# Kernel optimization log

Hardware: AMD Instinct MI355X
Metric: run time of the kernel (lower is better)

Reference implementation:

```python
import jax, jax.numpy as jnp
from jax import lax
import numpy as np

WAY = 100
SHOT = 5
QUERY = 15
D = 4096
LAM = 10.0
ALPHA = 0.2
N_EPOCHS = 20
EPS = 1e-6
MAXITERS = 1000
N_L = WAY * SHOT          # 500 labeled
N_U = WAY * QUERY         # 1500 unlabeled
N_TOT = N_L + N_U         # 2000


def setup_inputs() -> dict:
    key = jax.random.key(0)
    kx, = jax.random.split(key, 1)
    X = jax.random.uniform(kx, (N_TOT, D), dtype=jnp.float32)  # features must be >= 0
    # data is ordered as (shot+query) blocks of `way` samples, one per class
    labels = jnp.tile(jnp.arange(WAY, dtype=jnp.int32), SHOT + QUERY)
    return {"X": X, "labels": labels}


def _normalize(X):
    # F.normalize(p=2, dim=-1) with eps=1e-12
    return X / jnp.maximum(jnp.linalg.norm(X, axis=-1, keepdims=True), 1e-12)


def _cdist(X, Y):
    # Euclidean distances [n, m] via gram trick (avoids [n, m, d] intermediate)
    d2 = (X * X).sum(-1)[:, None] + (Y * Y).sum(-1)[None, :] - 2.0 * (X @ Y.T)
    return jnp.sqrt(jnp.maximum(d2, 1e-12))


def _sinkhorn(M, r, c):
    # Row/col scaling loop of compute_optimal_transport, tracked via scaling
    # vectors (a, b) so P_k = a * K * b exactly matches the in-place updates.
    K = jnp.exp(-LAM * M)
    K = K / K.sum()
    n, m = M.shape

    def step(carry, _):
        a, b, prev, done = carry
        rowsum = a * (K @ b)                       # P.sum(-1)
        err = jnp.max(jnp.abs(prev - rowsum))      # convergence check vs old u
        done = done | (err <= EPS)
        a_new = jnp.where(done, a, a * r / rowsum)
        colsum = b * (K.T @ a_new)                 # P.sum(1) after row scaling
        b_new = jnp.where(done, b, b * c / colsum)
        prev_new = jnp.where(done, prev, rowsum)
        return (a_new, b_new, prev_new, done), None

    init = (jnp.ones(n, M.dtype), jnp.ones(m, M.dtype),
            jnp.zeros(n, M.dtype), jnp.array(False))
    (a, b, _, _), _ = lax.scan(step, init, None, length=MAXITERS)
    return a[:, None] * K * b[None, :]


def _forward(X, labels):
    # power transform
    X = jnp.sqrt(X + 1e-6)
    # scale (mode='val'): normalize -> center labeled/unlabeled separately -> normalize
    X = _normalize(X)
    Xl = X[:N_L] - X[:N_L].mean(0, keepdims=True)
    Xu = X[N_L:] - X[N_L:].mean(0, keepdims=True)
    Z = _normalize(jnp.concatenate([Xl, Xu], axis=0))

    # init class means from labeled shots
    mus0 = Z.reshape(SHOT + QUERY, WAY, -1)[:SHOT].mean(0)  # [way, d]

    r = jnp.ones(N_U, Z.dtype)
    c = jnp.full((WAY,), float(QUERY), Z.dtype)
    onehot = jax.nn.one_hot(labels[:N_L], WAY, dtype=Z.dtype)

    def get_probas(mus):
        dist = _cdist(Z, mus)                      # [n_tot, way]
        Pu = _sinkhorn(dist[N_L:], r, c)           # [n_u, way]
        return jnp.concatenate([onehot, Pu], axis=0)

    def epoch(mus, _):
        p = get_probas(mus)
        emus = (p.T @ Z) / p.sum(0)[:, None]       # estimate_from_mask
        return mus + ALPHA * (emus - mus), None    # update_from_estimate

    mus, _ = lax.scan(epoch, mus0, None, length=N_EPOCHS)

    P = get_probas(mus)
    logP = jnp.log(P[N_L:] + 1e-5)
    acc = (jnp.argmax(P[N_L:], axis=-1) == labels[N_L:]).astype(jnp.float32).mean()
    return logP, acc


def reference(X, labels):
    return _forward(X, labels)
```

## Files before the change

### kernel.cpp

```cpp
#include <hip/hip_runtime.h>

#define WAY   100
#define SHOT  5
#define NQ    15
#define DD    4096
#define N_L   500
#define N_U   1500
#define N_TOT 2000
#define LAMF  10.0f
#define EPSF  1e-6f
#define MAXIT 1000

#define OFF_Z      0u
#define OFF_CPP    3145728u
#define OFF_MEANL  8192000u
#define OFF_MEANU  8196096u
#define OFF_SL     8200192u
#define OFF_MUSA   8609792u
#define OFF_MUSB   9068544u
#define OFF_MUSQP  9527296u
#define OFF_MUSB16 9552896u
#define OFF_PTH    9782272u
#define OFF_PTL    9868288u
#define OFF_KMAT   9954304u
#define OFF_COLS   10104320u
#define OFF_MISC   10113920u
#define OFF_ZUT    10114688u
#define OFF_ZUTL   13260416u
#define OFF_AG     16406144u
#define OFF_PREVG  16407680u
#define OFF_BINIT  16409216u

#define SINK_BLOCKS 8
#define SINK_T 512
#define RPB 188
#define KLS 101
#define PTS 1536
#define CPS 409600u

typedef __attribute__((ext_vector_type(8))) short short8_t;
typedef __attribute__((ext_vector_type(4))) float f32x4;

__device__ __forceinline__ short f2bs(float f) {
  unsigned u = __float_as_uint(f);
  unsigned r = (u + 0x7FFFu + ((u >> 16) & 1u)) >> 16;
  return (short)r;
}
__device__ __forceinline__ float bs2f(short s) {
  return __uint_as_float(((unsigned)(unsigned short)s) << 16);
}

__device__ __forceinline__ float ld_agent(const float* p) {
  return __hip_atomic_load(p, __ATOMIC_RELAXED, __HIP_MEMORY_SCOPE_AGENT);
}
__device__ __forceinline__ void st_agent(float* p, float v) {
  __hip_atomic_store(p, v, __ATOMIC_RELAXED, __HIP_MEMORY_SCOPE_AGENT);
}

__global__ __launch_bounds__(256) void k_pow_norm(const float* __restrict__ X, float* __restrict__ Z,
                                                  float* __restrict__ msums, unsigned* __restrict__ misc_u,
                                                  float* __restrict__ aG) {
  int i = blockIdx.x, tid = threadIdx.x;
  __shared__ float red[256];
  if (i < 32) msums[i * 256 + tid] = 0.f;
  if (i == 32) { misc_u[tid] = 0u; misc_u[tid + 256] = 0u; misc_u[tid + 512] = 0u; }
  if (i == 33) { for (int z = tid; z < 1504; z += 256) aG[z] = -1.f; }
  const float* x = X + (size_t)i * DD;
  float s = 0.f;
  for (int k = tid; k < DD; k += 256) s += x[k] + 1e-6f;
  red[tid] = s; __syncthreads();
  for (int o = 128; o > 0; o >>= 1) { if (tid < o) red[tid] += red[tid + o]; __syncthreads(); }
  float inv = 1.0f / fmaxf(sqrtf(red[0]), 1e-12f);
  float* z = Z + (size_t)i * DD;
  for (int k = tid; k < DD; k += 256) z[k] = sqrtf(x[k] + 1e-6f) * inv;
}

__global__ __launch_bounds__(256) void k_colmeans(const float* __restrict__ Z, float* __restrict__ mLs,
                                                  float* __restrict__ mUs) {
  int k = blockIdx.x * 256 + threadIdx.x;
  int r0 = blockIdx.y * 80;
  float sL = 0.f, sU = 0.f;
  for (int r = r0; r < r0 + 80; ++r) {
    float v = Z[(size_t)r * DD + k];
    if (r < N_L) sL += v; else sU += v;
  }
  if (r0 < N_L) atomicAdd(&mLs[k], sL);
  if (r0 + 80 > N_L) atomicAdd(&mUs[k], sU);
}

__global__ __launch_bounds__(256) void k_center(float* __restrict__ Z, const float* __restrict__ mLs,
                                                const float* __restrict__ mUs) {
  int i = blockIdx.x, tid = threadIdx.x;
  __shared__ float red[256];
  const float* m = (i < N_L) ? mLs : mUs;
  const float scale = (i < N_L) ? (1.0f / 500.0f) : (1.0f / 1500.0f);
  float* z = Z + (size_t)i * DD;
  float s = 0.f;
  for (int k = tid; k < DD; k += 256) { float v = z[k] - m[k] * scale; s += v * v; }
  red[tid] = s; __syncthreads();
  for (int o = 128; o > 0; o >>= 1) { if (tid < o) red[tid] += red[tid + o]; __syncthreads(); }
  float inv = 1.0f / fmaxf(sqrtf(red[0]), 1e-12f);
  for (int k = tid; k < DD; k += 256) z[k] = (z[k] - m[k] * scale) * inv;
}

__global__ __launch_bounds__(256) void k_musinit(const float* __restrict__ Z, float* __restrict__ SL,
                                                 float* __restrict__ mus, short* __restrict__ musb,
                                                 float* __restrict__ musqP, float* __restrict__ binit) {
  int w = blockIdx.x, tid = threadIdx.x;
  __shared__ float red[256];
  if (tid == 0) binit[w] = 1.0f;
  float q = 0.f;
  for (int k = tid; k < DD; k += 256) {
    float s = 0.f;
    for (int sh = 0; sh < SHOT; ++sh) s += Z[(size_t)(sh * WAY + w) * DD + k];
    SL[(size_t)w * DD + k] = s;
    float m = s / 5.0f;
    mus[(size_t)w * DD + k] = m;
    musb[(size_t)w * DD + k] = f2bs(m);
    q += m * m;
  }
  red[tid] = q; __syncthreads();
  for (int o = 128; o > 0; o >>= 1) { if (tid < o) red[tid] += red[tid + o]; __syncthreads(); }
  if (tid == 0) musqP[(size_t)w * 256] = red[0];
  else musqP[(size_t)w * 256 + tid] = 0.f;
}

__global__ __launch_bounds__(256) void k_zb(const float* __restrict__ Z, short* __restrict__ Zb, int ubase) {
  size_t i0 = (size_t)ubase * DD + ((size_t)blockIdx.x * 256 + threadIdx.x) * 8;
  short8_t v;
  if (i0 < (size_t)N_U * DD) {
    const float* src = Z + (size_t)N_L * DD + i0;
    float4 a = *(const float4*)src;
    float4 b = *(const float4*)(src + 4);
    v[0] = f2bs(a.x); v[1] = f2bs(a.y); v[2] = f2bs(a.z); v[3] = f2bs(a.w);
    v[4] = f2bs(b.x); v[5] = f2bs(b.y); v[6] = f2bs(b.z); v[7] = f2bs(b.w);
  } else {
    v = (short8_t){0, 0, 0, 0, 0, 0, 0, 0};
  }
  *(short8_t*)(Zb + i0) = v;
}

__global__ __launch_bounds__(256) void k_zt(const float* __restrict__ Z, short* __restrict__ ZTH,
                                            short* __restrict__ ZTL) {
  __shared__ float tile[32][33];
  int k0 = blockIdx.x * 32, u0 = blockIdx.y * 32;
  int c = threadIdx.x & 31, r0 = threadIdx.x >> 5;
#pragma unroll
  for (int rr = 0; rr < 4; ++rr) {
    int r = r0 + rr * 8;
    int u = u0 + r;
    tile[r][c] = (u < N_U) ? Z[(size_t)(N_L + u) * DD + k0 + c] : 0.f;
  }
  __syncthreads();
#pragma unroll
  for (int rr = 0; rr < 4; ++rr) {
    int r = r0 + rr * 8;
    float v = tile[c][r];
    short hi = f2bs(v);
    ZTH[(size_t)(k0 + r) * PTS + u0 + c] = hi;
    ZTL[(size_t)(k0 + r) * PTS + u0 + c] = f2bs(v - bs2f(hi));
  }
}

__global__ __launch_bounds__(256) void k_gemm1K(const short* __restrict__ Zb, const short* __restrict__ musb,
                                                const float* __restrict__ musqP, float* __restrict__ Kmat,
                                                unsigned* __restrict__ misc_u) {
  int tid = threadIdx.x;
  __shared__ float redA[4 * 7 * 4 * 64];
  __shared__ float musq2[2][128];
  if (blockIdx.x == 0) {
    for (int z = tid; z < 768; z += 256) misc_u[z] = 0u;
  }
  {
    int w = tid >> 1, half = tid & 1;
    if (w < WAY) {
      const float* mp = musqP + (size_t)w * 256 + half * 128;
      float q = 0.f;
#pragma unroll 4
      for (int bb = 0; bb < 128; bb += 4) {
        float4 v4 = *(const float4*)(mp + bb);
        q += (v4.x + v4.y) + (v4.z + v4.w);
      }
      musq2[half][w] = q;
    }
  }
  int wv = tid >> 6, l = tid & 63;
  int l15 = l & 15, quad = (l >> 4) & 3;
  int u0 = blockIdx.x * 16;
  f32x4 acc[7];
#pragma unroll
  for (int c = 0; c < 7; ++c) acc[c] = (f32x4){0.f, 0.f, 0.f, 0.f};

  const short* bp = Zb + (size_t)(u0 + l15) * DD + wv * 1024 + quad * 8;
  const short* ap = musb + (size_t)l15 * DD + wv * 1024 + quad * 8;
#pragma unroll 2
  for (int kc = 0; kc < 1024; kc += 32) {
    short8_t bf = *(const short8_t*)(bp + kc);
#pragma unroll
    for (int c = 0; c < 7; ++c) {
      short8_t af = *(const short8_t*)(ap + (size_t)c * 16 * DD + kc);
      acc[c] = __builtin_amdgcn_mfma_f32_16x16x32_bf16(af, bf, acc[c], 0, 0, 0);
    }
  }
#pragma unroll
  for (int c = 0; c < 7; ++c)
#pragma unroll
    for (int r = 0; r < 4; ++r)
      redA[((wv * 7 + c) * 4 + r) * 64 + l] = acc[c][r];
  __syncthreads();
  if (wv == 0) {
    int u = u0 + l15;
#pragma unroll
    for (int c = 0; c < 7; ++c)
#pragma unroll
      for (int r = 0; r < 4; ++r) {
        int base = (c * 4 + r) * 64 + l;
        float s = redA[base] + redA[base + 1792] + redA[base + 3584] + redA[base + 5376];
        int w = 16 * c + quad * 4 + r;
        if (w < WAY && u < N_U) {
          float d2 = 1.0f + (musq2[0][w] + musq2[1][w]) - 2.0f * s;
          Kmat[(size_t)u * WAY + w] = expf(-LAMF * sqrtf(fmaxf(d2, 1e-12f)));
        }
      }
  }
}

__device__ __forceinline__ void gbar(unsigned* slots, unsigned t) {
  __syncthreads();
  if (threadIdx.x == 0) {
    asm volatile("s_waitcnt vmcnt(0) lgkmcnt(0)" ::: "memory");
    __hip_atomic_store(slots + (unsigned)blockIdx.x * 16, t, __ATOMIC_RELAXED, __HIP_MEMORY_SCOPE_AGENT);
  }
  if (threadIdx.x < SINK_BLOCKS) {
    while (__hip_atomic_load(slots + threadIdx.x * 16, __ATOMIC_RELAXED, __HIP_MEMORY_SCOPE_AGENT) < t)
      __builtin_amdgcn_s_sleep(1);
  }
  __syncthreads();
}

__global__ __launch_bounds__(SINK_T) void k_sink(const float* __restrict__ Kg,
                                                 short* __restrict__ PTH, short* __restrict__ PTL,
                                                 float* __restrict__ colsP, float* __restrict__ aG,
                                                 float* __restrict__ prevG, float* __restrict__ binit,
                                                 unsigned* __restrict__ misc_u, float* __restrict__ misc_f) {
  __shared__ float Kl[RPB * KLS];
  __shared__ float a[RPB], aold[RPB], prevs[RPB], b[WAY];
  __shared__ float rerr[SINK_T];
  __shared__ float c2[5 * WAY];
  __shared__ float red[SINK_T];
  __shared__ float eSh;
  unsigned* slots = misc_u + 8;
  float* KsumG = misc_f + 3;
  int tid = threadIdx.x;
  int row0 = blockIdx.x * RPB;
  int nrows = (row0 + RPB <= N_U) ? RPB : (N_U - row0);

  float ks = 0.f;
  for (int idx = tid; idx < nrows * WAY; idx += SINK_T) {
    float v = Kg[row0 * WAY + idx];
    int r = idx / WAY, j = idx - r * WAY;
    Kl[r * KLS + j] = v;
    ks += v;
  }
  red[tid] = ks; __syncthreads();
  for (int o = SINK_T / 2; o > 0; o >>= 1) { if (tid < o) red[tid] += red[tid + o]; __syncthreads(); }
  if (tid == 0) atomicAdd(KsumG, red[0]);
  if (tid < WAY) b[tid] = binit[tid];

  bool warm = (aG[row0] >= 0.f);
  unsigned bt = 0;
  if (!warm) { ++bt; gbar(slots, bt); }
  float S = warm ? 1.f : ld_agent(KsumG);
  if (tid < RPB) {
    a[tid] = warm ? aG[row0 + tid] : (1.0f / S);
    prevs[tid] = warm ? prevG[row0 + tid] : 0.f;
  }

  bool conv = false;
  for (int t = 0; t < MAXIT; ++t) {
    float* cp = colsP + (t & 1) * 4096;
    __syncthreads();
    if (tid < nrows) {
      const float* kr = &Kl[tid * KLS];
      float r0 = 0.f, r1 = 0.f, r2 = 0.f, r3 = 0.f;
#pragma unroll 4
      for (int j = 0; j < WAY; j += 4) {
        r0 = fmaf(kr[j], b[j], r0);
        r1 = fmaf(kr[j + 1], b[j + 1], r1);
        r2 = fmaf(kr[j + 2], b[j + 2], r2);
        r3 = fmaf(kr[j + 3], b[j + 3], r3);
      }
      float rs = ((r0 + r1) + (r2 + r3)) * a[tid];
      rerr[tid] = fabsf(prevs[tid] - rs);
      aold[tid] = a[tid];
      a[tid] = a[tid] / rs;
      prevs[tid] = rs;
    } else {
      rerr[tid] = 0.f;
    }
    __syncthreads();
    if (tid < 500) {
      int slot = tid / 100;
      int j = tid - slot * 100;
      int rlo = slot * 38;
      int rhi = rlo + 38; if (rhi > nrows) rhi = nrows;
      float pc = 0.f;
      for (int r = rlo; r < rhi; ++r) pc = fmaf(Kl[r * KLS + j], a[r], pc);
      c2[slot * WAY + j] = pc;
    }
    __syncthreads();
    if (tid < WAY) {
      float s0 = c2[tid] + c2[WAY + tid] + c2[2 * WAY + tid] + c2[3 * WAY + tid] + c2[4 * WAY + tid];
      st_agent(cp + (unsigned)blockIdx.x * 128 + tid, s0);
    }
    if (tid < 64) {
      float m = rerr[tid];
#pragma unroll
      for (int k = 1; k < 8; ++k) m = fmaxf(m, rerr[tid + 64 * k]);
#pragma unroll
      for (int o = 32; o > 0; o >>= 1) m = fmaxf(m, __shfl_down(m, o));
      if (tid == 0) st_agent(cp + (unsigned)blockIdx.x * 128 + 100, m);
    }
    ++bt;
    gbar(slots, bt);
    float bnew = 0.f;
    if (tid >= 256 && tid < 256 + WAY) {
      int j = tid - 256;
      float s = 0.f;
#pragma unroll
      for (int sb = 0; sb < SINK_BLOCKS; ++sb) s += ld_agent(cp + sb * 128 + j);
      bnew = (float)NQ / s;
    }
    if (tid < 64) {
      float e = (tid < SINK_BLOCKS) ? ld_agent(cp + tid * 128 + 100) : 0.f;
#pragma unroll
      for (int o = 4; o > 0; o >>= 1) e = fmaxf(e, __shfl_down(e, o));
      if (tid == 0) eSh = e;
    }
    __syncthreads();
    if (eSh <= EPSF) { conv = true; break; }
    if (tid >= 256 && tid < 256 + WAY) b[tid - 256] = bnew;
  }
  __syncthreads();
  if (tid < nrows) {
    float af = conv ? aold[tid] : a[tid];
    aG[row0 + tid] = af;
    prevG[row0 + tid] = prevs[tid];
  }
  if (blockIdx.x == 0 && tid < WAY) binit[tid] = b[tid];
  for (int idx = tid; idx < WAY * nrows; idx += SINK_T) {
    int j = idx / nrows; int r = idx - j * nrows;
    float av = conv ? aold[r] : a[r];
    float p = av * Kl[r * KLS + j] * b[j];
    short hi = f2bs(p);
    PTH[(size_t)j * PTS + row0 + r] = hi;
    PTL[(size_t)j * PTS + row0 + r] = f2bs(p - bs2f(hi));
  }
  if (blockIdx.x == SINK_BLOCKS - 1) {
    for (int idx = tid; idx < WAY * 4; idx += SINK_T) {
      int j = idx >> 2;
      PTH[(size_t)j * PTS + 1500 + (idx & 3)] = 0;
      PTL[(size_t)j * PTS + 1500 + (idx & 3)] = 0;
    }
  }
}

__global__ __launch_bounds__(64) void k_gemm2(const short* __restrict__ PTH, const short* __restrict__ PTL,
                                              const short* __restrict__ ZTH, const short* __restrict__ ZTL,
                                              float* __restrict__ CPp) {
  int l = threadIdx.x, l15 = l & 15, quad = l >> 4;
  int k0 = blockIdx.x * 16;
  int us = blockIdx.y;
  int kcb = us * 192;
  int kce = (us == 7) ? 1504 : kcb + 192;
  f32x4 acc[7];
#pragma unroll
  for (int c = 0; c < 7; ++c) acc[c] = (f32x4){0.f, 0.f, 0.f, 0.f};
  size_t aoff = (size_t)l15 * PTS + quad * 8;
  const short* bph = ZTH + (size_t)(k0 + l15) * PTS + quad * 8;
  const short* bpl = ZTL + (size_t)(k0 + l15) * PTS + quad * 8;
  for (int kc = kcb; kc < kce; kc += 32) {
    short8_t bh = *(const short8_t*)(bph + kc);
    short8_t bl = *(const short8_t*)(bpl + kc);
#pragma unroll
    for (int c = 0; c < 7; ++c) {
      short8_t ah = *(const short8_t*)(PTH + aoff + (size_t)c * 16 * PTS + kc);
      short8_t al = *(const short8_t*)(PTL + aoff + (size_t)c * 16 * PTS + kc);
      acc[c] = __builtin_amdgcn_mfma_f32_16x16x32_bf16(ah, bh, acc[c], 0, 0, 0);
      acc[c] = __builtin_amdgcn_mfma_f32_16x16x32_bf16(al, bh, acc[c], 0, 0, 0);
      acc[c] = __builtin_amdgcn_mfma_f32_16x16x32_bf16(ah, bl, acc[c], 0, 0, 0);
    }
  }
  float* dst = CPp + (size_t)us * CPS;
#pragma unroll
  for (int c = 0; c < 7; ++c)
#pragma unroll
    for (int r = 0; r < 4; ++r) {
      int w = 16 * c + quad * 4 + r;
      if (w < WAY) dst[(size_t)w * DD + k0 + l15] = acc[c][r];
    }
}

__global__ __launch_bounds__(256) void k_musup(const float* __restrict__ musR, const float* __restrict__ SL,
                                               const float* __restrict__ CPp, float* __restrict__ musW,
                                               short* __restrict__ musb, float* __restrict__ musqP) {
  int w = blockIdx.x, tid = threadIdx.x;
  int kb = blockIdx.y * 1024;
  __shared__ float red[256];
  float q = 0.f;
  for (int k = kb + tid; k < kb + 1024; k += 256) {
    size_t o = (size_t)w * DD + k;
    float c = 0.f;
#pragma unroll
    for (int s = 0; s < 8; ++s) c += CPp[(size_t)s * CPS + o];
    float emus = (SL[o] + c) / 20.0f;
    float m = musR[o];
    float v = m + 0.2f * (emus - m);
    musW[o] = v;
    musb[o] = f2bs(v);
    q += v * v;
  }
  red[tid] = q; __syncthreads();
  for (int o = 128; o > 0; o >>= 1) { if (tid < o) red[tid] += red[tid + o]; __syncthreads(); }
  if (tid == 0) musqP[(size_t)w * 256 + blockIdx.y] = red[0];
}

__global__ __launch_bounds__(128) void k_final(const short* __restrict__ PTH, const short* __restrict__ PTL,
                                               const int* __restrict__ labels, float* __restrict__ out,
                                               unsigned* __restrict__ ctr) {
  int u = blockIdx.x, tid = threadIdx.x;
  __shared__ float vals[WAY];
  if (tid < WAY) {
    float v = bs2f(PTH[(size_t)tid * PTS + u]) + bs2f(PTL[(size_t)tid * PTS + u]);
    vals[tid] = v;
    out[(size_t)u * WAY + tid] = logf(v + 1e-5f);
  }
  __syncthreads();
  if (tid == 0) {
    int am = 0; float bv = vals[0];
    for (int j = 1; j < WAY; ++j) { if (vals[j] > bv) { bv = vals[j]; am = j; } }
    if (am == labels[N_L + u]) atomicAdd(ctr, 1u);
  }
}

__global__ void k_acc(const unsigned* __restrict__ ctr, float* __restrict__ out) {
  if (threadIdx.x == 0) out[N_U * WAY] = (float)(*ctr) / 1500.0f;
}

extern "C" void kernel_launch(void* const* d_in, const int* in_sizes, int n_in,
                              void* d_out, int out_size, void* d_ws, size_t ws_size,
                              hipStream_t stream) {
  const float* X = (const float*)d_in[0];
  const int* labels = (const int*)d_in[1];
  float* out = (float*)d_out;
  float* ws = (float*)d_ws;

  float* Z     = ws + OFF_Z;
  short* Zb    = (short*)(ws + OFF_Z);
  float* CPp   = ws + OFF_CPP;
  float* meanL = ws + OFF_MEANL;
  float* meanU = ws + OFF_MEANU;
  float* SL    = ws + OFF_SL;
  float* musA  = ws + OFF_MUSA;
  float* musB  = ws + OFF_MUSB;
  float* musqP = ws + OFF_MUSQP;
  short* musb16 = (short*)(ws + OFF_MUSB16);
  short* PTH   = (short*)(ws + OFF_PTH);
  short* PTL   = (short*)(ws + OFF_PTL);
  float* Kmat  = ws + OFF_KMAT;
  float* colsP = ws + OFF_COLS;
  float* misc_f = ws + OFF_MISC;
  unsigned* misc_u = (unsigned*)(ws + OFF_MISC);
  short* ZTH   = (short*)(ws + OFF_ZUT);
  short* ZTL   = (short*)(ws + OFF_ZUTL);
  float* aG    = ws + OFF_AG;
  float* prevG = ws + OFF_PREVG;
  float* binit = ws + OFF_BINIT;

  k_pow_norm<<<N_TOT, 256, 0, stream>>>(X, Z, meanL, misc_u, aG);
  k_colmeans<<<dim3(16, 25), 256, 0, stream>>>(Z, meanL, meanU);
  k_center<<<N_TOT, 256, 0, stream>>>(Z, meanL, meanU);
  k_musinit<<<WAY, 256, 0, stream>>>(Z, SL, musA, musb16, musqP, binit);
  k_zt<<<dim3(128, 48), 256, 0, stream>>>(Z, ZTH, ZTL);
  k_zb<<<1536, 256, 0, stream>>>(Z, Zb, 0);
  k_zb<<<1536, 256, 0, stream>>>(Z, Zb, 768);

  float* musR = musA;
  float* musW = musB;
  for (int e = 0; e < 20; ++e) {
    k_gemm1K<<<96, 256, 0, stream>>>(Zb, musb16, musqP, Kmat, misc_u);
    k_sink<<<SINK_BLOCKS, SINK_T, 0, stream>>>(Kmat, PTH, PTL, colsP, aG, prevG, binit, misc_u, misc_f);
    k_gemm2<<<dim3(256, 8), 64, 0, stream>>>(PTH, PTL, ZTH, ZTL, CPp);
    k_musup<<<dim3(WAY, 4), 256, 0, stream>>>(musR, SL, CPp, musW, musb16, musqP);
    float* tmp = musR; musR = musW; musW = tmp;
  }
  k_gemm1K<<<96, 256, 0, stream>>>(Zb, musb16, musqP, Kmat, misc_u);
  k_sink<<<SINK_BLOCKS, SINK_T, 0, stream>>>(Kmat, PTH, PTL, colsP, aG, prevG, binit, misc_u, misc_f);
  k_final<<<N_U, 128, 0, stream>>>(PTH, PTL, labels, out, misc_u + 5);
  k_acc<<<1, 64, 0, stream>>>(misc_u + 5, out);
}
```

Before: 2.313 ms.

## Split Sinkhorn over 16 blocks, fuse gemm2 with mus update and final output

The Sinkhorn solver now runs on 16 cooperating blocks of 94 rows instead of 8 blocks of 188, and its inner loops use float4 shared-memory accesses. The split-K GEMM plus separate mus-update kernel is replaced by one full-K MFMA kernel that applies the update and norm partials directly, which removes the CPp partial buffer round trip. The final log/argmax kernel is folded into the last Sinkhorn launch. Using more blocks shortens the per-iteration row work but adds participants to the spin barrier, and the full-K GEMM runs only 256 blocks.

```diff
diff --git a/kernel.cpp b/kernel.cpp
--- a/kernel.cpp
+++ b/kernel.cpp
@@ -12,7 +12,6 @@
 #define MAXIT 1000
 
 #define OFF_Z      0u
-#define OFF_CPP    3145728u
 #define OFF_MEANL  8192000u
 #define OFF_MEANU  8196096u
 #define OFF_SL     8200192u
@@ -31,12 +30,11 @@
 #define OFF_PREVG  16407680u
 #define OFF_BINIT  16409216u
 
-#define SINK_BLOCKS 8
+#define SINK_BLOCKS 16
 #define SINK_T 512
-#define RPB 188
-#define KLS 101
+#define RPB 94
+#define CPR 12
 #define PTS 1536
-#define CPS 409600u
 
 typedef __attribute__((ext_vector_type(8))) short short8_t;
 typedef __attribute__((ext_vector_type(4))) float f32x4;
@@ -232,7 +230,7 @@
     __hip_atomic_store(slots + (unsigned)blockIdx.x * 16, t, __ATOMIC_RELAXED, __HIP_MEMORY_SCOPE_AGENT);
   }
   if (threadIdx.x < SINK_BLOCKS) {
-    while (__hip_atomic_load(slots + threadIdx.x * 16, __ATOMIC_RELAXED, __HIP_MEMORY_SCOPE_AGENT) < t)
+    while (__hip_atomic_load(slots + threadIdx.x * 16, __ATOMIC_ACQUIRE, __HIP_MEMORY_SCOPE_AGENT) < t)
       __builtin_amdgcn_s_sleep(1);
   }
   __syncthreads();
@@ -242,55 +240,60 @@
                                                  short* __restrict__ PTH, short* __restrict__ PTL,
                                                  float* __restrict__ colsP, float* __restrict__ aG,
                                                  float* __restrict__ prevG, float* __restrict__ binit,
-                                                 unsigned* __restrict__ misc_u, float* __restrict__ misc_f) {
-  __shared__ float Kl[RPB * KLS];
-  __shared__ float a[RPB], aold[RPB], prevs[RPB], b[WAY];
+                                                 unsigned* __restrict__ misc_u, float* __restrict__ misc_f,
+                                                 const int* __restrict__ labels, float* __restrict__ out,
+                                                 int finalmode) {
+  __shared__ float Kl[RPB * 100];
+  __shared__ float4 bS4[25];
+  __shared__ float a[RPB], aold[RPB], prevs[RPB];
   __shared__ float rerr[SINK_T];
-  __shared__ float c2[5 * WAY];
+  __shared__ float c2[800];
   __shared__ float red[SINK_T];
   __shared__ float eSh;
+  float* bS = (float*)bS4;
   unsigned* slots = misc_u + 8;
   float* KsumG = misc_f + 3;
   int tid = threadIdx.x;
-  int row0 = blockIdx.x * RPB;
-  int nrows = (row0 + RPB <= N_U) ? RPB : (N_U - row0);
+  int row0 = (int)blockIdx.x * RPB;
+  int nrows = (blockIdx.x == SINK_BLOCKS - 1) ? (N_U - row0) : RPB;
 
   float ks = 0.f;
-  for (int idx = tid; idx < nrows * WAY; idx += SINK_T) {
-    float v = Kg[row0 * WAY + idx];
-    int r = idx / WAY, j = idx - r * WAY;
-    Kl[r * KLS + j] = v;
-    ks += v;
+  int n4 = nrows * 25;
+  const float4* Ksrc = (const float4*)(Kg + (size_t)row0 * 100);
+  for (int i = tid; i < n4; i += SINK_T) {
+    float4 v = Ksrc[i];
+    *(float4*)(&Kl[i * 4]) = v;
+    ks += (v.x + v.y) + (v.z + v.w);
   }
   red[tid] = ks; __syncthreads();
   for (int o = SINK_T / 2; o > 0; o >>= 1) { if (tid < o) red[tid] += red[tid + o]; __syncthreads(); }
   if (tid == 0) atomicAdd(KsumG, red[0]);
-  if (tid < WAY) b[tid] = binit[tid];
+  if (tid < WAY) bS[tid] = binit[tid];
 
   bool warm = (aG[row0] >= 0.f);
   unsigned bt = 0;
   if (!warm) { ++bt; gbar(slots, bt); }
   float S = warm ? 1.f : ld_agent(KsumG);
-  if (tid < RPB) {
+  if (tid < nrows) {
     a[tid] = warm ? aG[row0 + tid] : (1.0f / S);
     prevs[tid] = warm ? prevG[row0 + tid] : 0.f;
   }
 
   bool conv = false;
   for (int t = 0; t < MAXIT; ++t) {
-    float* cp = colsP + (t & 1) * 4096;
+    float* cp = colsP + (t & 1) * 2048;
     __syncthreads();
     if (tid < nrows) {
-      const float* kr = &Kl[tid * KLS];
-      float r0 = 0.f, r1 = 0.f, r2 = 0.f, r3 = 0.f;
-#pragma unroll 4
-      for (int j = 0; j < WAY; j += 4) {
-        r0 = fmaf(kr[j], b[j], r0);
-        r1 = fmaf(kr[j + 1], b[j + 1], r1);
-        r2 = fmaf(kr[j + 2], b[j + 2], r2);
-        r3 = fmaf(kr[j + 3], b[j + 3], r3);
+      const float* kr = &Kl[tid * 100];
+      float4 ac = {0.f, 0.f, 0.f, 0.f};
+#pragma unroll
+      for (int j4 = 0; j4 < 25; ++j4) {
+        float4 bv = bS4[j4];
+        float4 kv = *(const float4*)(kr + j4 * 4);
+        ac.x = fmaf(kv.x, bv.x, ac.x); ac.y = fmaf(kv.y, bv.y, ac.y);
+        ac.z = fmaf(kv.z, bv.z, ac.z); ac.w = fmaf(kv.w, bv.w, ac.w);
       }
-      float rs = ((r0 + r1) + (r2 + r3)) * a[tid];
+      float rs = ((ac.x + ac.y) + (ac.z + ac.w)) * a[tid];
       rerr[tid] = fabsf(prevs[tid] - rs);
       aold[tid] = a[tid];
       a[tid] = a[tid] / rs;
@@ -299,27 +302,32 @@
       rerr[tid] = 0.f;
     }
     __syncthreads();
-    if (tid < 500) {
-      int slot = tid / 100;
-      int j = tid - slot * 100;
-      int rlo = slot * 38;
-      int rhi = rlo + 38; if (rhi > nrows) rhi = nrows;
-      float pc = 0.f;
-      for (int r = rlo; r < rhi; ++r) pc = fmaf(Kl[r * KLS + j], a[r], pc);
-      c2[slot * WAY + j] = pc;
+    if (tid < 200) {
+      int j4 = tid % 25, ch = tid / 25;
+      int rlo = ch * CPR, rhi = rlo + CPR; if (rhi > nrows) rhi = nrows;
+      float4 pa = {0.f, 0.f, 0.f, 0.f};
+      for (int r = rlo; r < rhi; ++r) {
+        float4 kv = *(const float4*)(&Kl[r * 100 + j4 * 4]);
+        float av = a[r];
+        pa.x = fmaf(kv.x, av, pa.x); pa.y = fmaf(kv.y, av, pa.y);
+        pa.z = fmaf(kv.z, av, pa.z); pa.w = fmaf(kv.w, av, pa.w);
+      }
+      *(float4*)(&c2[ch * 100 + j4 * 4]) = pa;
+    }
+    if (tid >= 448) {
+      int t6 = tid & 63;
+      float m = rerr[t6];
+#pragma unroll
+      for (int k = 1; k < 8; ++k) m = fmaxf(m, rerr[t6 + 64 * k]);
+#pragma unroll
+      for (int o = 32; o > 0; o >>= 1) m = fmaxf(m, __shfl_down(m, o));
+      if (t6 == 0) st_agent(cp + (unsigned)blockIdx.x * 128 + 100, m);
     }
     __syncthreads();
     if (tid < WAY) {
-      float s0 = c2[tid] + c2[WAY + tid] + c2[2 * WAY + tid] + c2[3 * WAY + tid] + c2[4 * WAY + tid];
-      st_agent(cp + (unsigned)blockIdx.x * 128 + tid, s0);
-    }
-    if (tid < 64) {
-      float m = rerr[tid];
-#pragma unroll
-      for (int k = 1; k < 8; ++k) m = fmaxf(m, rerr[tid + 64 * k]);
-#pragma unroll
-      for (int o = 32; o > 0; o >>= 1) m = fmaxf(m, __shfl_down(m, o));
-      if (tid == 0) st_agent(cp + (unsigned)blockIdx.x * 128 + 100, m);
+      float s = ((c2[tid] + c2[100 + tid]) + (c2[200 + tid] + c2[300 + tid])) +
+                ((c2[400 + tid] + c2[500 + tid]) + (c2[600 + tid] + c2[700 + tid]));
+      st_agent(cp + (unsigned)blockIdx.x * 128 + tid, s);
     }
     ++bt;
     gbar(slots, bt);
@@ -334,24 +342,41 @@
     if (tid < 64) {
       float e = (tid < SINK_BLOCKS) ? ld_agent(cp + tid * 128 + 100) : 0.f;
 #pragma unroll
-      for (int o = 4; o > 0; o >>= 1) e = fmaxf(e, __shfl_down(e, o));
+      for (int o = 8; o > 0; o >>= 1) e = fmaxf(e, __shfl_down(e, o));
       if (tid == 0) eSh = e;
     }
     __syncthreads();
     if (eSh <= EPSF) { conv = true; break; }
-    if (tid >= 256 && tid < 256 + WAY) b[tid - 256] = bnew;
+    if (tid >= 256 && tid < 256 + WAY) bS[tid - 256] = bnew;
   }
   __syncthreads();
+
+  if (finalmode) {
+    for (int idx = tid; idx < nrows * WAY; idx += SINK_T) {
+      int r = idx / WAY, j = idx - r * WAY;
+      float av = conv ? aold[r] : a[r];
+      float p = av * Kl[r * 100 + j] * bS[j];
+      out[(size_t)(row0 + r) * WAY + j] = logf(p + 1e-5f);
+    }
+    if (tid < nrows) {
+      const float* kr = &Kl[tid * 100];
+      int am = 0; float bv = kr[0] * bS[0];
+      for (int j = 1; j < WAY; ++j) { float p = kr[j] * bS[j]; if (p > bv) { bv = p; am = j; } }
+      if (am == labels[N_L + row0 + tid]) atomicAdd(misc_u + 5, 1u);
+    }
+    return;
+  }
+
   if (tid < nrows) {
     float af = conv ? aold[tid] : a[tid];
     aG[row0 + tid] = af;
     prevG[row0 + tid] = prevs[tid];
   }
-  if (blockIdx.x == 0 && tid < WAY) binit[tid] = b[tid];
+  if (blockIdx.x == 0 && tid < WAY) binit[tid] = bS[tid];
   for (int idx = tid; idx < WAY * nrows; idx += SINK_T) {
     int j = idx / nrows; int r = idx - j * nrows;
     float av = conv ? aold[r] : a[r];
-    float p = av * Kl[r * KLS + j] * b[j];
+    float p = av * Kl[r * 100 + j] * bS[j];
     short hi = f2bs(p);
     PTH[(size_t)j * PTS + row0 + r] = hi;
     PTL[(size_t)j * PTS + row0 + r] = f2bs(p - bs2f(hi));
@@ -365,81 +390,63 @@
   }
 }
 
-__global__ __launch_bounds__(64) void k_gemm2(const short* __restrict__ PTH, const short* __restrict__ PTL,
-                                              const short* __restrict__ ZTH, const short* __restrict__ ZTL,
-                                              float* __restrict__ CPp) {
-  int l = threadIdx.x, l15 = l & 15, quad = l >> 4;
-  int k0 = blockIdx.x * 16;
-  int us = blockIdx.y;
-  int kcb = us * 192;
-  int kce = (us == 7) ? 1504 : kcb + 192;
-  f32x4 acc[7];
-#pragma unroll
-  for (int c = 0; c < 7; ++c) acc[c] = (f32x4){0.f, 0.f, 0.f, 0.f};
-  size_t aoff = (size_t)l15 * PTS + quad * 8;
-  const short* bph = ZTH + (size_t)(k0 + l15) * PTS + quad * 8;
-  const short* bpl = ZTL + (size_t)(k0 + l15) * PTS + quad * 8;
-  for (int kc = kcb; kc < kce; kc += 32) {
+__global__ __launch_bounds__(128) void k_gemm2m(const short* __restrict__ PTH, const short* __restrict__ PTL,
+                                                const short* __restrict__ ZTH, const short* __restrict__ ZTL,
+                                                const float* __restrict__ musR, const float* __restrict__ SL,
+                                                float* __restrict__ musW, short* __restrict__ musb,
+                                                float* __restrict__ musqP) {
+  int tid = threadIdx.x, wv = tid >> 6, l = tid & 63;
+  int l15 = l & 15, quad = (l >> 4) & 3;
+  int k0 = blockIdx.x;
+  int c0 = wv ? 4 : 0, nc = wv ? 3 : 4;
+  __shared__ float sq2[7][16][16];
+  f32x4 acc[4];
+#pragma unroll
+  for (int c = 0; c < 4; ++c) acc[c] = (f32x4){0.f, 0.f, 0.f, 0.f};
+  size_t aoff = (size_t)(c0 * 16 + l15) * PTS + quad * 8;
+  const short* bph = ZTH + (size_t)(k0 * 16 + l15) * PTS + quad * 8;
+  const short* bpl = ZTL + (size_t)(k0 * 16 + l15) * PTS + quad * 8;
+  for (int kc = 0; kc < 1504; kc += 32) {
     short8_t bh = *(const short8_t*)(bph + kc);
     short8_t bl = *(const short8_t*)(bpl + kc);
 #pragma unroll
-    for (int c = 0; c < 7; ++c) {
-      short8_t ah = *(const short8_t*)(PTH + aoff + (size_t)c * 16 * PTS + kc);
-      short8_t al = *(const short8_t*)(PTL + aoff + (size_t)c * 16 * PTS + kc);
-      acc[c] = __builtin_amdgcn_mfma_f32_16x16x32_bf16(ah, bh, acc[c], 0, 0, 0);
-      acc[c] = __builtin_amdgcn_mfma_f32_16x16x32_bf16(al, bh, acc[c], 0, 0, 0);
-      acc[c] = __builtin_amdgcn_mfma_f32_16x16x32_bf16(ah, bl, acc[c], 0, 0, 0);
-    }
-  }
-  float* dst = CPp + (size_t)us * CPS;
-#pragma unroll
-  for (int c = 0; c < 7; ++c)
-#pragma unroll
-    for (int r = 0; r < 4; ++r) {
-      int w = 16 * c + quad * 4 + r;
-      if (w < WAY) dst[(size_t)w * DD + k0 + l15] = acc[c][r];
-    }
-}
-
-__global__ __launch_bounds__(256) void k_musup(const float* __restrict__ musR, const float* __restrict__ SL,
-                                               const float* __restrict__ CPp, float* __restrict__ musW,
-                                               short* __restrict__ musb, float* __restrict__ musqP) {
-  int w = blockIdx.x, tid = threadIdx.x;
-  int kb = blockIdx.y * 1024;
-  __shared__ float red[256];
-  float q = 0.f;
-  for (int k = kb + tid; k < kb + 1024; k += 256) {
-    size_t o = (size_t)w * DD + k;
-    float c = 0.f;
-#pragma unroll
-    for (int s = 0; s < 8; ++s) c += CPp[(size_t)s * CPS + o];
-    float emus = (SL[o] + c) / 20.0f;
-    float m = musR[o];
-    float v = m + 0.2f * (emus - m);
-    musW[o] = v;
-    musb[o] = f2bs(v);
-    q += v * v;
-  }
-  red[tid] = q; __syncthreads();
-  for (int o = 128; o > 0; o >>= 1) { if (tid < o) red[tid] += red[tid + o]; __syncthreads(); }
-  if (tid == 0) musqP[(size_t)w * 256 + blockIdx.y] = red[0];
-}
-
-__global__ __launch_bounds__(128) void k_final(const short* __restrict__ PTH, const short* __restrict__ PTL,
-                                               const int* __restrict__ labels, float* __restrict__ out,
-                                               unsigned* __restrict__ ctr) {
-  int u = blockIdx.x, tid = threadIdx.x;
-  __shared__ float vals[WAY];
+    for (int c = 0; c < 4; ++c) {
+      if (c < nc) {
+        short8_t ah = *(const short8_t*)(PTH + aoff + (size_t)c * 16 * PTS + kc);
+        short8_t al = *(const short8_t*)(PTL + aoff + (size_t)c * 16 * PTS + kc);
+        acc[c] = __builtin_amdgcn_mfma_f32_16x16x32_bf16(ah, bh, acc[c], 0, 0, 0);
+        acc[c] = __builtin_amdgcn_mfma_f32_16x16x32_bf16(al, bh, acc[c], 0, 0, 0);
+        acc[c] = __builtin_amdgcn_mfma_f32_16x16x32_bf16(ah, bl, acc[c], 0, 0, 0);
+      }
+    }
+  }
+  int kk = k0 * 16 + l15;
+#pragma unroll
+  for (int c = 0; c < 4; ++c) {
+    if (c < nc) {
+#pragma unroll
+      for (int r = 0; r < 4; ++r) {
+        int w = (c0 + c) * 16 + quad * 4 + r;
+        float vsq = 0.f;
+        if (w < WAY) {
+          size_t o = (size_t)w * DD + kk;
+          float emus = (SL[o] + acc[c][r]) / 20.0f;
+          float m = musR[o];
+          float v = m + 0.2f * (emus - m);
+          musW[o] = v;
+          musb[o] = f2bs(v);
+          vsq = v * v;
+        }
+        sq2[c0 + c][quad * 4 + r][l15] = vsq;
+      }
+    }
+  }
+  __syncthreads();
   if (tid < WAY) {
-    float v = bs2f(PTH[(size_t)tid * PTS + u]) + bs2f(PTL[(size_t)tid * PTS + u]);
-    vals[tid] = v;
-    out[(size_t)u * WAY + tid] = logf(v + 1e-5f);
-  }
-  __syncthreads();
-  if (tid == 0) {
-    int am = 0; float bv = vals[0];
-    for (int j = 1; j < WAY; ++j) { if (vals[j] > bv) { bv = vals[j]; am = j; } }
-    if (am == labels[N_L + u]) atomicAdd(ctr, 1u);
+    float s = 0.f;
+#pragma unroll
+    for (int i = 0; i < 16; ++i) s += sq2[tid >> 4][tid & 15][i];
+    musqP[(size_t)tid * 256 + k0] = s;
   }
 }
 
@@ -457,7 +464,6 @@
 
   float* Z     = ws + OFF_Z;
   short* Zb    = (short*)(ws + OFF_Z);
-  float* CPp   = ws + OFF_CPP;
   float* meanL = ws + OFF_MEANL;
   float* meanU = ws + OFF_MEANU;
   float* SL    = ws + OFF_SL;
@@ -489,13 +495,13 @@
   float* musW = musB;
   for (int e = 0; e < 20; ++e) {
     k_gemm1K<<<96, 256, 0, stream>>>(Zb, musb16, musqP, Kmat, misc_u);
-    k_sink<<<SINK_BLOCKS, SINK_T, 0, stream>>>(Kmat, PTH, PTL, colsP, aG, prevG, binit, misc_u, misc_f);
-    k_gemm2<<<dim3(256, 8), 64, 0, stream>>>(PTH, PTL, ZTH, ZTL, CPp);
-    k_musup<<<dim3(WAY, 4), 256, 0, stream>>>(musR, SL, CPp, musW, musb16, musqP);
+    k_sink<<<SINK_BLOCKS, SINK_T, 0, stream>>>(Kmat, PTH, PTL, colsP, aG, prevG, binit, misc_u, misc_f,
+                                               labels, out, 0);
+    k_gemm2m<<<256, 128, 0, stream>>>(PTH, PTL, ZTH, ZTL, musR, SL, musW, musb16, musqP);
     float* tmp = musR; musR = musW; musW = tmp;
   }
   k_gemm1K<<<96, 256, 0, stream>>>(Zb, musb16, musqP, Kmat, misc_u);
-  k_sink<<<SINK_BLOCKS, SINK_T, 0, stream>>>(Kmat, PTH, PTL, colsP, aG, prevG, binit, misc_u, misc_f);
-  k_final<<<N_U, 128, 0, stream>>>(PTH, PTL, labels, out, misc_u + 5);
+  k_sink<<<SINK_BLOCKS, SINK_T, 0, stream>>>(Kmat, PTH, PTL, colsP, aG, prevG, binit, misc_u, misc_f,
+                                             labels, out, 1);
   k_acc<<<1, 64, 0, stream>>>(misc_u + 5, out);
 }
```

Measured after the change: 2.456 ms. 1.06x slower.
